# Kernel optimization log

Measured on AMD Instinct MI355X. Metric: run time of the kernel, lower is better.

The kernel has to match this reference:

```python
import jax, jax.numpy as jnp
import numpy as np

NA = 40000   # author nodes
NP = 40000   # paper nodes
E = 800000   # edges per relation
HID = 64
HOP = 5
SEM = 128


def setup_inputs() -> dict:
    key = jax.random.key(0)
    ks = jax.random.split(key, 32)
    f32 = jnp.float32
    rn = lambda k, s, sc=0.1: jax.random.normal(k, s, f32) * sc
    inp = {}
    inp["x_author"] = jax.random.normal(ks[0], (NA, 334), f32)
    inp["x_paper"] = jax.random.normal(ks[1], (NP, 512), f32)
    inp["W1_a"] = rn(ks[2], (334, HID), 0.05)
    inp["b1_a"] = jnp.zeros((HID,), f32)
    inp["W1_p"] = rn(ks[3], (512, HID), 0.05)
    inp["b1_p"] = jnp.zeros((HID,), f32)
    inp["a1_ap"] = rn(ks[4], (HOP, HID))
    inp["a2_ap"] = rn(ks[5], (HOP, HID))
    inp["a1_aa"] = rn(ks[6], (HOP, HID))
    inp["a2_aa"] = rn(ks[7], (HOP, HID))
    inp["a1_pa"] = rn(ks[8], (HOP, HID))
    inp["a2_pa"] = rn(ks[9], (HOP, HID))
    inp["a1_pp"] = rn(ks[10], (HOP, HID))
    inp["a2_pp"] = rn(ks[11], (HOP, HID))
    inp["semW_a"] = rn(ks[12], (HOP, HID, SEM))
    inp["semb_a"] = jnp.zeros((HOP, SEM), f32)
    inp["semq_a"] = rn(ks[13], (HOP, SEM))
    inp["semW_p"] = rn(ks[14], (HOP, HID, SEM))
    inp["semb_p"] = jnp.zeros((HOP, SEM), f32)
    inp["semq_p"] = rn(ks[15], (HOP, SEM))
    inp["W2"] = rn(ks[16], (HID, 4))
    inp["b2"] = jnp.zeros((4,), f32)
    inp["ei_ap"] = jax.random.randint(ks[17], (2, E), 0, NA)  # row0=src(author) row1=tgt(paper)
    inp["ei_aa"] = jax.random.randint(ks[18], (2, E), 0, NA)
    inp["ei_pa"] = jax.random.randint(ks[19], (2, E), 0, NP)
    inp["ei_pp"] = jax.random.randint(ks[20], (2, E), 0, NP)
    return inp


def _leaky(v):
    return jnp.where(v > 0.0, v, 0.2 * v)


def _edge_agg(x, h, s, t, a1, a2, n):
    # x: [Ns,D] source features (fixed), h: [Nt,D] current target state
    x1 = x @ a1                                   # [Ns]
    h1 = h @ a2                                   # [Nt]
    w2 = jnp.exp(_leaky(x1 + x @ a2))             # [Ns] self-loop score
    w1 = jnp.exp(_leaky(x1[s] + h1[t]))           # [E]  edge score
    div = jax.ops.segment_sum(w1, s, num_segments=n) + w2
    num = jax.ops.segment_sum(w1[:, None] * h[t], s, num_segments=n) + w2[:, None] * x
    return num / div[:, None]


def _sem(z, W, b, q):
    # z: [N,M,D]; HAN-style semantic attention over M relations
    sc = jnp.tanh(jnp.einsum('nmd,dk->nmk', z, W) + b) @ q   # [N,M]
    beta = jax.nn.softmax(jnp.mean(sc, axis=0))               # [M]
    return jnp.einsum('m,nmd->nd', beta, z)


def reference(x_author, x_paper, W1_a, b1_a, W1_p, b1_p,
              a1_ap, a2_ap, a1_aa, a2_aa, a1_pa, a2_pa, a1_pp, a2_pp,
              semW_a, semb_a, semq_a, semW_p, semb_p, semq_p,
              W2, b2, ei_ap, ei_aa, ei_pa, ei_pp):
    # eval mode: dropout is identity
    xA = jax.nn.relu(x_author @ W1_a + b1_a)
    xP = jax.nn.relu(x_paper @ W1_p + b1_p)
    hA, hP = xA, xP
    nA, nP = xA.shape[0], xP.shape[0]
    for i in range(HOP):
        eA = jnp.stack([
            _edge_agg(xA, hP, ei_ap[0], ei_ap[1], a1_ap[i], a2_ap[i], nA),
            _edge_agg(xA, hA, ei_aa[0], ei_aa[1], a1_aa[i], a2_aa[i], nA)], axis=1)
        eP = jnp.stack([
            _edge_agg(xP, hA, ei_pa[0], ei_pa[1], a1_pa[i], a2_pa[i], nP),
            _edge_agg(xP, hP, ei_pp[0], ei_pp[1], a1_pp[i], a2_pp[i], nP)], axis=1)
        hA = jax.nn.elu(_sem(eA, semW_a[i], semb_a[i], semq_a[i]))
        hP = jax.nn.elu(_sem(eP, semW_p[i], semb_p[i], semq_p[i]))
    return hA @ W2 + b2   # target_node_type = 'author'
```

## Files before the change

### kernel.cpp

```cpp
#include <hip/hip_runtime.h>
#include <hip/hip_fp16.h>

#define NN 40000
#define DD 64
#define EE 800000
#define NHOP 5
#define NSEM 128
#define NBK 625
#define BINCH 8192

__device__ __forceinline__ float leaky02(float v) { return v > 0.f ? v : 0.2f * v; }
__device__ __forceinline__ float tanh_fast(float x) {
  return 1.f - 2.f / (__expf(2.f * x) + 1.f);
}
__device__ __forceinline__ float wred(float x) {
  #pragma unroll
  for (int m = 1; m < 64; m <<= 1) x += __shfl_xor(x, m);
  return x;
}

__global__ void zero_i32(int* __restrict__ p, int n) {
  int i = blockIdx.x * blockDim.x + threadIdx.x;
  if (i < n) p[i] = 0;
}

#define PBM 64
#define PBK 64
__global__ __launch_bounds__(512) void proj_gemm_relu(
    const float* __restrict__ X, const float* __restrict__ W,
    const float* __restrict__ bias, float* __restrict__ out,
    __half* __restrict__ out16, int n, int K)
{
  __shared__ float As[PBM][PBK + 1];
  __shared__ float Bs[PBK][DD];
  int tid = threadIdx.x;
  int tx = tid & 15;
  int ty = tid >> 4;
  int row0 = blockIdx.x * PBM;
  float acc[2][4] = {{0.f}};
  int nk = (K + PBK - 1) / PBK;
  for (int kt = 0; kt < nk; ++kt) {
    int k0 = kt * PBK;
    #pragma unroll
    for (int j = 0; j < 8; ++j) {
      int idx = tid + j * 512;
      int r = idx >> 6, c = idx & 63;
      int gk = k0 + c;
      As[r][c] = (gk < K) ? X[(size_t)(row0 + r) * K + gk] : 0.f;
    }
    #pragma unroll
    for (int j = 0; j < 2; ++j) {
      int idx = tid + j * 512;
      int r = idx >> 4, c4 = idx & 15;
      int gk = k0 + r;
      float4 v = (gk < K) ? ((const float4*)(W + (size_t)gk * DD))[c4]
                          : make_float4(0.f, 0.f, 0.f, 0.f);
      ((float4*)&Bs[r][0])[c4] = v;
    }
    __syncthreads();
    #pragma unroll 8
    for (int kk = 0; kk < PBK; ++kk) {
      float a0 = As[ty * 2][kk];
      float a1 = As[ty * 2 + 1][kk];
      float4 bv = ((float4*)&Bs[kk][0])[tx];
      acc[0][0] = fmaf(a0, bv.x, acc[0][0]);
      acc[0][1] = fmaf(a0, bv.y, acc[0][1]);
      acc[0][2] = fmaf(a0, bv.z, acc[0][2]);
      acc[0][3] = fmaf(a0, bv.w, acc[0][3]);
      acc[1][0] = fmaf(a1, bv.x, acc[1][0]);
      acc[1][1] = fmaf(a1, bv.y, acc[1][1]);
      acc[1][2] = fmaf(a1, bv.z, acc[1][2]);
      acc[1][3] = fmaf(a1, bv.w, acc[1][3]);
    }
    __syncthreads();
  }
  float4 bb = ((const float4*)bias)[tx];
  #pragma unroll
  for (int i = 0; i < 2; ++i) {
    int gr = row0 + ty * 2 + i;
    float4 v;
    v.x = fmaxf(acc[i][0] + bb.x, 0.f);
    v.y = fmaxf(acc[i][1] + bb.y, 0.f);
    v.z = fmaxf(acc[i][2] + bb.z, 0.f);
    v.w = fmaxf(acc[i][3] + bb.w, 0.f);
    ((float4*)(out + (size_t)gr * DD))[tx] = v;
    __half2 p0 = __floats2half2_rn(v.x, v.y);
    __half2 p1 = __floats2half2_rn(v.z, v.w);
    ((__half2*)(out16 + (size_t)gr * DD))[tx * 2 + 0] = p0;
    ((__half2*)(out16 + (size_t)gr * DD))[tx * 2 + 1] = p1;
  }
}

__global__ __launch_bounds__(256) void binCount_kernel(
    const int* __restrict__ e0, const int* __restrict__ e1,
    const int* __restrict__ e2, const int* __restrict__ e3,
    int* __restrict__ bcnt, int e)
{
  int rel = blockIdx.y;
  const int* S = rel == 0 ? e0 : rel == 1 ? e1 : rel == 2 ? e2 : e3;
  __shared__ int cnt[NBK];
  int tid = threadIdx.x;
  for (int b = tid; b < NBK; b += 256) cnt[b] = 0;
  __syncthreads();
  int e0i = blockIdx.x * BINCH;
  int ne = min(BINCH, e - e0i);
  for (int i = tid; i < ne; i += 256) atomicAdd(&cnt[S[e0i + i] >> 6], 1);
  __syncthreads();
  for (int b = tid; b < NBK; b += 256)
    if (cnt[b]) atomicAdd(&bcnt[rel * NBK + b], cnt[b]);
}

__global__ __launch_bounds__(1024) void bucketScan_kernel(
    const int* __restrict__ bcnt, int* __restrict__ bbase, int* __restrict__ bcur,
    int* __restrict__ rp0, int* __restrict__ rp1, int* __restrict__ rp2,
    int* __restrict__ rp3, int e)
{
  int rel = blockIdx.x;
  __shared__ int sh[1024];
  int t = threadIdx.x;
  int v = (t < NBK) ? bcnt[rel * NBK + t] : 0;
  sh[t] = v;
  __syncthreads();
  for (int off = 1; off < 1024; off <<= 1) {
    int y = (t >= off) ? sh[t - off] : 0;
    __syncthreads();
    sh[t] += y;
    __syncthreads();
  }
  if (t < NBK) {
    int base = sh[t] - v;
    bbase[rel * (NBK + 1) + t] = base;
    bcur[rel * NBK + t] = base;
  }
  if (t == 0) {
    bbase[rel * (NBK + 1) + NBK] = e;
    (rel == 0 ? rp0 : rel == 1 ? rp1 : rel == 2 ? rp2 : rp3)[NN] = e;
  }
}

__global__ __launch_bounds__(256) void binA_kernel(
    const int* __restrict__ e0, const int* __restrict__ e1,
    const int* __restrict__ e2, const int* __restrict__ e3,
    int* __restrict__ bcur, unsigned* __restrict__ pairbuf, int e)
{
  int rel = blockIdx.y;
  const int* S = rel == 0 ? e0 : rel == 1 ? e1 : rel == 2 ? e2 : e3;
  const int* T = S + e;
  unsigned* pb = pairbuf + (size_t)rel * e;
  __shared__ int cnt[NBK], base[NBK], cnt2[NBK];
  int tid = threadIdx.x;
  for (int b = tid; b < NBK; b += 256) { cnt[b] = 0; cnt2[b] = 0; }
  __syncthreads();
  int e0i = blockIdx.x * BINCH;
  int ne = min(BINCH, e - e0i);
  for (int i = tid; i < ne; i += 256) atomicAdd(&cnt[S[e0i + i] >> 6], 1);
  __syncthreads();
  for (int b = tid; b < NBK; b += 256)
    base[b] = cnt[b] ? atomicAdd(&bcur[rel * NBK + b], cnt[b]) : 0;
  __syncthreads();
  for (int i = tid; i < ne; i += 256) {
    int s = S[e0i + i];
    int t = T[e0i + i];
    int b = s >> 6;
    int off = atomicAdd(&cnt2[b], 1);
    pb[base[b] + off] = ((unsigned)(s & 63) << 16) | (unsigned)t;
  }
}

__global__ __launch_bounds__(256) void binB_kernel(
    const unsigned* __restrict__ pairbuf, const int* __restrict__ bbase,
    int* __restrict__ rp0, int* __restrict__ rp1, int* __restrict__ rp2,
    int* __restrict__ rp3,
    unsigned short* __restrict__ ts0, unsigned short* __restrict__ ts1,
    unsigned short* __restrict__ ts2, unsigned short* __restrict__ ts3, int e)
{
  int rel = blockIdx.y;
  int* rowptr = rel == 0 ? rp0 : rel == 1 ? rp1 : rel == 2 ? rp2 : rp3;
  unsigned short* ts = rel == 0 ? ts0 : rel == 1 ? ts1 : rel == 2 ? ts2 : ts3;
  const unsigned* pb = pairbuf + (size_t)rel * e;
  int b = blockIdx.x;
  int bstart = bbase[rel * (NBK + 1) + b];
  int bend   = bbase[rel * (NBK + 1) + b + 1];
  __shared__ int ncnt[64], cur[64];
  int tid = threadIdx.x;
  if (tid < 64) ncnt[tid] = 0;
  __syncthreads();
  for (int i = bstart + tid; i < bend; i += 256)
    atomicAdd(&ncnt[(pb[i] >> 16) & 63], 1);
  __syncthreads();
  if (tid < 64) {
    int v = ncnt[tid];
    int x = v;
    #pragma unroll
    for (int off = 1; off < 64; off <<= 1) {
      int y = __shfl_up(x, off);
      if (tid >= off) x += y;
    }
    int nb = bstart + x - v;
    rowptr[b * 64 + tid] = nb;
    cur[tid] = nb;
  }
  __syncthreads();
  for (int i = bstart + tid; i < bend; i += 256) {
    unsigned u = pb[i];
    int pos = atomicAdd(&cur[(u >> 16) & 63], 1);
    ts[pos] = (unsigned short)(u & 0xffffu);
  }
}

__global__ __launch_bounds__(256) void precompute_xw(
    const float* __restrict__ xA, const float* __restrict__ xP,
    const float* __restrict__ a1_ap, const float* __restrict__ a2_ap,
    const float* __restrict__ a1_aa, const float* __restrict__ a2_aa,
    const float* __restrict__ a1_pa, const float* __restrict__ a2_pa,
    const float* __restrict__ a1_pp, const float* __restrict__ a2_pp,
    float* __restrict__ x1all, float* __restrict__ w2all,
    float* __restrict__ h1_ap, float* __restrict__ h1_aa,
    float* __restrict__ h1_pa, float* __restrict__ h1_pp)
{
  int side = blockIdx.y;
  __shared__ float L[21 * DD];
  int tid = threadIdx.x;
  {
    const float* s0 = side ? a1_pa : a1_ap;
    const float* s1 = side ? a2_pa : a2_ap;
    const float* s2 = side ? a1_pp : a1_aa;
    const float* s3 = side ? a2_pp : a2_aa;
    const float* ex = side ? a2_ap : a2_pa;
    for (int i = tid; i < 21 * DD; i += 256) {
      int k = i >> 6, d = i & 63;
      const float* src = (k < 5) ? s0 : (k < 10) ? s1 : (k < 15) ? s2 : (k < 20) ? s3 : ex;
      int hop = (k < 20) ? (k % 5) : 0;
      L[i] = src[hop * DD + d];
    }
  }
  __syncthreads();
  int j = blockIdx.x * 256 + tid;
  if (j >= NN) return;
  const float4* x4 = (const float4*)((side ? xP : xA) + (size_t)j * DD);
  float acc[21];
  #pragma unroll
  for (int k = 0; k < 21; ++k) acc[k] = 0.f;
  #pragma unroll
  for (int d0 = 0; d0 < 16; ++d0) {
    float4 v = x4[d0];
    #pragma unroll
    for (int c = 0; c < 4; ++c) {
      int d = d0 * 4 + c;
      float xv = (&v.x)[c];
      #pragma unroll
      for (int k = 0; k < 21; ++k) acc[k] = fmaf(xv, L[k * DD + d], acc[k]);
    }
  }
  int relA = side ? 2 : 0;
  #pragma unroll
  for (int i = 0; i < NHOP; ++i) {
    x1all[((size_t)(relA + 0) * NHOP + i) * NN + j] = acc[0 * 5 + i];
    w2all[((size_t)(relA + 0) * NHOP + i) * NN + j] =
        __expf(leaky02(acc[0 * 5 + i] + acc[1 * 5 + i]));
    x1all[((size_t)(relA + 1) * NHOP + i) * NN + j] = acc[2 * 5 + i];
    w2all[((size_t)(relA + 1) * NHOP + i) * NN + j] =
        __expf(leaky02(acc[2 * 5 + i] + acc[3 * 5 + i]));
  }
  if (side) { h1_pp[j] = acc[15]; h1_ap[j] = acc[20]; }
  else      { h1_aa[j] = acc[15]; h1_pa[j] = acc[20]; }
}

struct AggRel {
  const float* x; const __half2* h2; const float* x1; const float* w2; const float* h1;
  const int* rowptr; const unsigned short* tsorted; float* out;
};

__global__ __launch_bounds__(256) void agg4_kernel(AggRel r0, AggRel r1, AggRel r2,
                                                   AggRel r3, int n)
{
  int bid = blockIdx.x;
  int g = (bid >> 2) & 1;
  int u = (bid >> 3) * 4 + (bid & 3);
  int half = n >> 2;
  int relsel = u >= half;
  int nodeblk = relsel ? (u - half) : u;
  AggRel R;
  if (g == 0) R = relsel ? r2 : r1;
  else        R = relsel ? r3 : r0;

  int wid = nodeblk * 4 + (threadIdx.x >> 6);
  int lane = threadIdx.x & 63;
  int pair = lane >> 5;
  int c2 = lane & 31;

  int beg = R.rowptr[wid], end = R.rowptr[wid + 1];
  float x1i = R.x1[wid];
  float2 accA = make_float2(0.f, 0.f), accB = make_float2(0.f, 0.f);
  float2 accC = make_float2(0.f, 0.f), accD = make_float2(0.f, 0.f);
  float wsumL = 0.f;
  for (int c = beg; c < end; c += 64) {
    int idx = c + lane;
    int t = 0;
    float wv = 0.f;
    if (idx < end) {
      t = R.tsorted[idx];
      wv = __expf(leaky02(x1i + R.h1[t]));
    }
    wsumL += wv;
    int ne = min(64, end - c);
    for (int j = 0; j < ne; j += 8) {
      int s0 = j + pair, s1 = j + 2 + pair, s2 = j + 4 + pair, s3 = j + 6 + pair;
      int t0 = __shfl(t, s0), t1 = __shfl(t, s1);
      int t2 = __shfl(t, s2), t3 = __shfl(t, s3);
      float w0 = __shfl(wv, s0), w1 = __shfl(wv, s1);
      float w2_ = __shfl(wv, s2), w3 = __shfl(wv, s3);
      float2 f0 = __half22float2(R.h2[((unsigned)t0 << 5) + c2]);
      float2 f1 = __half22float2(R.h2[((unsigned)t1 << 5) + c2]);
      float2 f2 = __half22float2(R.h2[((unsigned)t2 << 5) + c2]);
      float2 f3 = __half22float2(R.h2[((unsigned)t3 << 5) + c2]);
      accA.x = fmaf(w0, f0.x, accA.x);
      accA.y = fmaf(w0, f0.y, accA.y);
      accB.x = fmaf(w1, f1.x, accB.x);
      accB.y = fmaf(w1, f1.y, accB.y);
      accC.x = fmaf(w2_, f2.x, accC.x);
      accC.y = fmaf(w2_, f2.y, accC.y);
      accD.x = fmaf(w3, f3.x, accD.x);
      accD.y = fmaf(w3, f3.y, accD.y);
    }
  }
  float wsum = wred(wsumL);
  float2 acc;
  acc.x = (accA.x + accB.x) + (accC.x + accD.x);
  acc.y = (accA.y + accB.y) + (accC.y + accD.y);
  acc.x += __shfl_xor(acc.x, 32);
  acc.y += __shfl_xor(acc.y, 32);
  if (pair == 0) {
    float w2v = R.w2[wid];
    float inv = 1.f / (wsum + w2v);
    float2 xv = ((const float2*)(R.x + (size_t)wid * DD))[c2];
    float2 o;
    o.x = fmaf(w2v, xv.x, acc.x) * inv;
    o.y = fmaf(w2v, xv.y, acc.y) * inv;
    ((float2*)(R.out + (size_t)wid * DD))[c2] = o;
  }
}

__global__ __launch_bounds__(256) void sem_kernel(
    const float* __restrict__ eA0, const float* __restrict__ eA1,
    const float* __restrict__ eP0, const float* __restrict__ eP1,
    const float* __restrict__ Wa, const float* __restrict__ ba, const float* __restrict__ qa,
    const float* __restrict__ Wp, const float* __restrict__ bp, const float* __restrict__ qp,
    float* __restrict__ psums)
{
  int side = blockIdx.y;
  const float* e0 = side ? eP0 : eA0;
  const float* e1 = side ? eP1 : eA1;
  const float* W = side ? Wp : Wa;
  const float* b = side ? bp : ba;
  const float* q = side ? qp : qa;

  __shared__ float Ws[DD * NSEM];
  __shared__ float zt[2][DD][12];
  __shared__ float red0[256], red1[256];
  int tid = threadIdx.x;
  {
    const float4* W4 = (const float4*)W;
    float4* Ws4 = (float4*)Ws;
    #pragma unroll
    for (int j = 0; j < 8; ++j) Ws4[tid + j * 256] = W4[tid + j * 256];
  }
  int slot = tid >> 7;
  int k = tid & 127;
  float bk = b[k], qk = q[k];
  int base = blockIdx.x * 64;
  float sum0 = 0.f, sum1 = 0.f;
  for (int it = 0; it < 8; ++it) {
    #pragma unroll
    for (int j = 0; j < 4; ++j) {
      int idx = tid + j * 256;
      int d = idx & 63, m = (idx >> 6) & 1, nn = idx >> 7;
      zt[m][d][nn] = (m ? e1 : e0)[(size_t)(base + it * 8 + nn) * DD + d];
    }
    __syncthreads();
    float a0[4], a1[4];
    #pragma unroll
    for (int nn = 0; nn < 4; ++nn) { a0[nn] = bk; a1[nn] = bk; }
    #pragma unroll 8
    for (int d = 0; d < DD; ++d) {
      float w = Ws[d * NSEM + k];
      float4 za = *(const float4*)&zt[0][d][slot * 4];
      float4 zb = *(const float4*)&zt[1][d][slot * 4];
      a0[0] = fmaf(za.x, w, a0[0]);
      a0[1] = fmaf(za.y, w, a0[1]);
      a0[2] = fmaf(za.z, w, a0[2]);
      a0[3] = fmaf(za.w, w, a0[3]);
      a1[0] = fmaf(zb.x, w, a1[0]);
      a1[1] = fmaf(zb.y, w, a1[1]);
      a1[2] = fmaf(zb.z, w, a1[2]);
      a1[3] = fmaf(zb.w, w, a1[3]);
    }
    #pragma unroll
    for (int nn = 0; nn < 4; ++nn) {
      sum0 += tanh_fast(a0[nn]) * qk;
      sum1 += tanh_fast(a1[nn]) * qk;
    }
    __syncthreads();
  }
  red0[tid] = sum0;
  red1[tid] = sum1;
  __syncthreads();
  for (int off = 128; off; off >>= 1) {
    if (tid < off) { red0[tid] += red0[tid + off]; red1[tid] += red1[tid + off]; }
    __syncthreads();
  }
  if (tid == 0) {
    int idx = (side * gridDim.x + blockIdx.x) * 2;
    psums[idx + 0] = red0[0];
    psums[idx + 1] = red1[0];
  }
}

__global__ __launch_bounds__(256) void beta_kernel(const float* __restrict__ psums,
    float* __restrict__ beta, int nblk, float invn)
{
  __shared__ float s[4][256];
  int t = threadIdx.x;
  float a0 = 0.f, a1 = 0.f, p0 = 0.f, p1 = 0.f;
  for (int i = t; i < nblk; i += 256) {
    a0 += psums[i * 2];
    a1 += psums[i * 2 + 1];
    p0 += psums[(nblk + i) * 2];
    p1 += psums[(nblk + i) * 2 + 1];
  }
  s[0][t] = a0; s[1][t] = a1; s[2][t] = p0; s[3][t] = p1;
  __syncthreads();
  for (int off = 128; off; off >>= 1) {
    if (t < off) {
      s[0][t] += s[0][t + off]; s[1][t] += s[1][t + off];
      s[2][t] += s[2][t + off]; s[3][t] += s[3][t + off];
    }
    __syncthreads();
  }
  if (t == 0) {
    float m0 = s[0][0] * invn, m1 = s[1][0] * invn;
    float mx = fmaxf(m0, m1);
    float x0 = __expf(m0 - mx), x1 = __expf(m1 - mx);
    float inv = 1.f / (x0 + x1);
    beta[0] = x0 * inv; beta[1] = x1 * inv;
    m0 = s[2][0] * invn; m1 = s[3][0] * invn;
    mx = fmaxf(m0, m1);
    x0 = __expf(m0 - mx); x1 = __expf(m1 - mx);
    inv = 1.f / (x0 + x1);
    beta[2] = x0 * inv; beta[3] = x1 * inv;
  }
}

__global__ void combine2_kernel(const float4* __restrict__ eA0, const float4* __restrict__ eA1,
    const float4* __restrict__ eP0, const float4* __restrict__ eP1,
    const float* __restrict__ beta, float4* __restrict__ hA, float4* __restrict__ hP,
    __half2* __restrict__ hA16, __half2* __restrict__ hP16,
    const float* __restrict__ a2_ap_n, const float* __restrict__ a2_aa_n,
    const float* __restrict__ a2_pa_n, const float* __restrict__ a2_pp_n,
    float* __restrict__ h1_ap, float* __restrict__ h1_aa,
    float* __restrict__ h1_pa, float* __restrict__ h1_pp,
    int has_next, int nvec)
{
  int side = blockIdx.y;
  int i = blockIdx.x * 256 + threadIdx.x;
  if (i >= nvec) return;
  float b0 = beta[side * 2], b1 = beta[side * 2 + 1];
  float4 v0 = (side ? eP0 : eA0)[i];
  float4 v1 = (side ? eP1 : eA1)[i];
  float4 r;
  float t;
  t = b0 * v0.x + b1 * v1.x; r.x = t > 0.f ? t : (__expf(t) - 1.f);
  t = b0 * v0.y + b1 * v1.y; r.y = t > 0.f ? t : (__expf(t) - 1.f);
  t = b0 * v0.z + b1 * v1.z; r.z = t > 0.f ? t : (__expf(t) - 1.f);
  t = b0 * v0.w + b1 * v1.w; r.w = t > 0.f ? t : (__expf(t) - 1.f);
  (side ? hP : hA)[i] = r;
  (side ? hP16 : hA16)[i * 2 + 0] = __floats2half2_rn(r.x, r.y);
  (side ? hP16 : hA16)[i * 2 + 1] = __floats2half2_rn(r.z, r.w);
  if (has_next) {
    int col4 = i & 15;
    const float* ax = side ? a2_ap_n : a2_aa_n;
    const float* ay = side ? a2_pp_n : a2_pa_n;
    float4 a4 = ((const float4*)ax)[col4];
    float4 c4 = ((const float4*)ay)[col4];
    float rx = r.x * a4.x + r.y * a4.y + r.z * a4.z + r.w * a4.w;
    float ry = r.x * c4.x + r.y * c4.y + r.z * c4.z + r.w * c4.w;
    #pragma unroll
    for (int m = 1; m < 16; m <<= 1) {
      rx += __shfl_xor(rx, m);
      ry += __shfl_xor(ry, m);
    }
    if ((threadIdx.x & 15) == 0) {
      int row = i >> 4;
      if (side) { h1_ap[row] = rx; h1_pp[row] = ry; }
      else      { h1_aa[row] = rx; h1_pa[row] = ry; }
    }
  }
}

__global__ void final_kernel(const float* __restrict__ hA, const float* __restrict__ W2,
    const float* __restrict__ b2, float* __restrict__ out, int n)
{
  int j = blockIdx.x * blockDim.x + threadIdx.x;
  if (j >= n) return;
  float acc0 = b2[0], acc1 = b2[1], acc2 = b2[2], acc3 = b2[3];
  const float4* hrow = (const float4*)(hA + (size_t)j * DD);
  #pragma unroll
  for (int d4 = 0; d4 < 16; ++d4) {
    float4 v = hrow[d4];
    #pragma unroll
    for (int c = 0; c < 4; ++c) {
      int d = d4 * 4 + c;
      float vv = (&v.x)[c];
      acc0 = fmaf(vv, W2[d * 4 + 0], acc0);
      acc1 = fmaf(vv, W2[d * 4 + 1], acc1);
      acc2 = fmaf(vv, W2[d * 4 + 2], acc2);
      acc3 = fmaf(vv, W2[d * 4 + 3], acc3);
    }
  }
  ((float4*)out)[j] = make_float4(acc0, acc1, acc2, acc3);
}

extern "C" void kernel_launch(void* const* d_in, const int* in_sizes, int n_in,
                              void* d_out, int out_size, void* d_ws, size_t ws_size,
                              hipStream_t stream)
{
  const float* x_author = (const float*)d_in[0];
  const float* x_paper  = (const float*)d_in[1];
  const float* W1_a = (const float*)d_in[2];
  const float* b1_a = (const float*)d_in[3];
  const float* W1_p = (const float*)d_in[4];
  const float* b1_p = (const float*)d_in[5];
  const float* a1_ap = (const float*)d_in[6];
  const float* a2_ap = (const float*)d_in[7];
  const float* a1_aa = (const float*)d_in[8];
  const float* a2_aa = (const float*)d_in[9];
  const float* a1_pa = (const float*)d_in[10];
  const float* a2_pa = (const float*)d_in[11];
  const float* a1_pp = (const float*)d_in[12];
  const float* a2_pp = (const float*)d_in[13];
  const float* semW_a = (const float*)d_in[14];
  const float* semb_a = (const float*)d_in[15];
  const float* semq_a = (const float*)d_in[16];
  const float* semW_p = (const float*)d_in[17];
  const float* semb_p = (const float*)d_in[18];
  const float* semq_p = (const float*)d_in[19];
  const float* W2 = (const float*)d_in[20];
  const float* b2 = (const float*)d_in[21];
  const int* ei[4] = {(const int*)d_in[22], (const int*)d_in[23],
                      (const int*)d_in[24], (const int*)d_in[25]};

  char* w = (char*)d_ws;
  auto alloc = [&](size_t bytes) -> void* {
    void* p = (void*)w;
    w += (bytes + 255) & ~(size_t)255;
    return p;
  };
  const size_t matB = (size_t)NN * DD * sizeof(float);
  float* xA  = (float*)alloc(matB);
  float* xP  = (float*)alloc(matB);
  float* hA  = (float*)alloc(matB);
  float* hP  = (float*)alloc(matB);
  float* eA0 = (float*)alloc(matB);
  float* eA1 = (float*)alloc(matB);
  float* eP0 = (float*)alloc(matB);
  float* eP1 = (float*)alloc(matB);
  __half* xA16 = (__half*)alloc(matB / 2);
  __half* xP16 = (__half*)alloc(matB / 2);
  __half* hA16 = xA16;
  __half* hP16 = xP16;
  unsigned* pairbuf = (unsigned*)eA0;
  int* rowptr[4]; unsigned short* tsorted[4];
  for (int r = 0; r < 4; ++r) {
    rowptr[r]  = (int*)alloc((NN + 1) * sizeof(int));
    tsorted[r] = (unsigned short*)alloc((size_t)EE * sizeof(unsigned short));
  }
  int* bcnt  = (int*)alloc((size_t)4 * NBK * sizeof(int));
  int* bbase = (int*)alloc((size_t)4 * (NBK + 1) * sizeof(int));
  int* bcur  = (int*)alloc((size_t)4 * NBK * sizeof(int));
  float* x1all = (float*)alloc((size_t)4 * NHOP * NN * sizeof(float));
  float* w2all = (float*)alloc((size_t)4 * NHOP * NN * sizeof(float));
  float* h1b[4];
  for (int r = 0; r < 4; ++r) h1b[r] = (float*)alloc(NN * sizeof(float));
  float* psums = (float*)alloc((size_t)2 * NBK * 2 * sizeof(float));
  float* betab = (float*)alloc(64);

  proj_gemm_relu<<<NN / PBM, 512, 0, stream>>>(x_author, W1_a, b1_a, xA, xA16, NN, 334);
  proj_gemm_relu<<<NN / PBM, 512, 0, stream>>>(x_paper,  W1_p, b1_p, xP, xP16, NN, 512);

  const int NEB = (EE + BINCH - 1) / BINCH;
  zero_i32<<<(4 * NBK + 255) / 256, 256, 0, stream>>>(bcnt, 4 * NBK);
  binCount_kernel<<<dim3(NEB, 4), 256, 0, stream>>>(ei[0], ei[1], ei[2], ei[3], bcnt, EE);
  bucketScan_kernel<<<4, 1024, 0, stream>>>(bcnt, bbase, bcur,
      rowptr[0], rowptr[1], rowptr[2], rowptr[3], EE);
  binA_kernel<<<dim3(NEB, 4), 256, 0, stream>>>(
      ei[0], ei[1], ei[2], ei[3], bcur, pairbuf, EE);
  binB_kernel<<<dim3(NBK, 4), 256, 0, stream>>>(pairbuf, bbase,
      rowptr[0], rowptr[1], rowptr[2], rowptr[3],
      tsorted[0], tsorted[1], tsorted[2], tsorted[3], EE);

  precompute_xw<<<dim3((NN + 255) / 256, 2), 256, 0, stream>>>(
      xA, xP, a1_ap, a2_ap, a1_aa, a2_aa, a1_pa, a2_pa, a1_pp, a2_pp,
      x1all, w2all, h1b[0], h1b[1], h1b[2], h1b[3]);

  const int CVEC = NN * DD / 4;
  for (int i = 0; i < NHOP; ++i) {
    #define X1(r) (x1all + ((size_t)(r) * NHOP + i) * NN)
    #define W2P(r) (w2all + ((size_t)(r) * NHOP + i) * NN)
    AggRel r0 = {xA, (const __half2*)hP16, X1(0), W2P(0), h1b[0], rowptr[0], tsorted[0], eA0};
    AggRel r1 = {xA, (const __half2*)hA16, X1(1), W2P(1), h1b[1], rowptr[1], tsorted[1], eA1};
    AggRel r2 = {xP, (const __half2*)hA16, X1(2), W2P(2), h1b[2], rowptr[2], tsorted[2], eP0};
    AggRel r3 = {xP, (const __half2*)hP16, X1(3), W2P(3), h1b[3], rowptr[3], tsorted[3], eP1};
    agg4_kernel<<<NN, 256, 0, stream>>>(r0, r1, r2, r3, NN);

    sem_kernel<<<dim3(NN / 64, 2), 256, 0, stream>>>(
        eA0, eA1, eP0, eP1,
        semW_a + (size_t)i * DD * NSEM, semb_a + i * NSEM, semq_a + i * NSEM,
        semW_p + (size_t)i * DD * NSEM, semb_p + i * NSEM, semq_p + i * NSEM,
        psums);
    beta_kernel<<<1, 256, 0, stream>>>(psums, betab, NN / 64, 1.f / NN);

    int inext = (i + 1 < NHOP) ? (i + 1) : i;
    combine2_kernel<<<dim3((CVEC + 255) / 256, 2), 256, 0, stream>>>(
        (const float4*)eA0, (const float4*)eA1, (const float4*)eP0, (const float4*)eP1,
        betab, (float4*)hA, (float4*)hP, (__half2*)hA16, (__half2*)hP16,
        a2_ap + inext * DD, a2_aa + inext * DD, a2_pa + inext * DD, a2_pp + inext * DD,
        h1b[0], h1b[1], h1b[2], h1b[3], (i + 1 < NHOP) ? 1 : 0, CVEC);
  }

  final_kernel<<<(NN + 255) / 256, 256, 0, stream>>>(hA, W2, b2, (float*)d_out, NN);
}
```

Before: 988.2 us.

## Replace tiled projection GEMM with thread-per-row kernel merging both node types

The shared-memory tiled projection GEMM is replaced by a kernel where each thread computes one full 64-wide output row. The thread reads its input row with vector loads and reads W rows as broadcast loads. Both author and paper projections now run in a single launch over a 2D grid. This drops LDS staging and a launch, but each thread streams its own strided row of X with no coalescing across threads and holds 64 accumulators, so memory efficiency and occupancy may suffer.

```diff
diff --git a/kernel.cpp b/kernel.cpp
--- a/kernel.cpp
+++ b/kernel.cpp
@@ -24,71 +24,64 @@
   if (i < n) p[i] = 0;
 }
 
-#define PBM 64
-#define PBK 64
-__global__ __launch_bounds__(512) void proj_gemm_relu(
+template <int VEC>
+__device__ __forceinline__ void proj_tpn_body(
     const float* __restrict__ X, const float* __restrict__ W,
     const float* __restrict__ bias, float* __restrict__ out,
-    __half* __restrict__ out16, int n, int K)
-{
-  __shared__ float As[PBM][PBK + 1];
-  __shared__ float Bs[PBK][DD];
-  int tid = threadIdx.x;
-  int tx = tid & 15;
-  int ty = tid >> 4;
-  int row0 = blockIdx.x * PBM;
-  float acc[2][4] = {{0.f}};
-  int nk = (K + PBK - 1) / PBK;
-  for (int kt = 0; kt < nk; ++kt) {
-    int k0 = kt * PBK;
-    #pragma unroll
-    for (int j = 0; j < 8; ++j) {
-      int idx = tid + j * 512;
-      int r = idx >> 6, c = idx & 63;
-      int gk = k0 + c;
-      As[r][c] = (gk < K) ? X[(size_t)(row0 + r) * K + gk] : 0.f;
-    }
-    #pragma unroll
-    for (int j = 0; j < 2; ++j) {
-      int idx = tid + j * 512;
-      int r = idx >> 4, c4 = idx & 15;
-      int gk = k0 + r;
-      float4 v = (gk < K) ? ((const float4*)(W + (size_t)gk * DD))[c4]
-                          : make_float4(0.f, 0.f, 0.f, 0.f);
-      ((float4*)&Bs[r][0])[c4] = v;
-    }
-    __syncthreads();
-    #pragma unroll 8
-    for (int kk = 0; kk < PBK; ++kk) {
-      float a0 = As[ty * 2][kk];
-      float a1 = As[ty * 2 + 1][kk];
-      float4 bv = ((float4*)&Bs[kk][0])[tx];
-      acc[0][0] = fmaf(a0, bv.x, acc[0][0]);
-      acc[0][1] = fmaf(a0, bv.y, acc[0][1]);
-      acc[0][2] = fmaf(a0, bv.z, acc[0][2]);
-      acc[0][3] = fmaf(a0, bv.w, acc[0][3]);
-      acc[1][0] = fmaf(a1, bv.x, acc[1][0]);
-      acc[1][1] = fmaf(a1, bv.y, acc[1][1]);
-      acc[1][2] = fmaf(a1, bv.z, acc[1][2]);
-      acc[1][3] = fmaf(a1, bv.w, acc[1][3]);
-    }
-    __syncthreads();
-  }
-  float4 bb = ((const float4*)bias)[tx];
+    __half* __restrict__ out16, int K, int j)
+{
+  const float* xrow = X + (size_t)j * K;
+  float acc[DD];
   #pragma unroll
-  for (int i = 0; i < 2; ++i) {
-    int gr = row0 + ty * 2 + i;
+  for (int o = 0; o < DD; ++o) acc[o] = 0.f;
+  for (int k = 0; k < K; k += VEC) {
+    float xv[VEC];
+    if (VEC == 4) {
+      float4 t = *(const float4*)(xrow + k);
+      xv[0] = t.x; xv[1] = t.y; xv[2] = t.z; xv[3] = t.w;
+    } else {
+      float2 t = *(const float2*)(xrow + k);
+      xv[0] = t.x; xv[1] = t.y;
+    }
+    #pragma unroll
+    for (int c = 0; c < VEC; ++c) {
+      const float4* wrow = (const float4*)(W + (size_t)(k + c) * DD);
+      #pragma unroll
+      for (int o4 = 0; o4 < 16; ++o4) {
+        float4 wv = wrow[o4];
+        acc[o4 * 4 + 0] = fmaf(xv[c], wv.x, acc[o4 * 4 + 0]);
+        acc[o4 * 4 + 1] = fmaf(xv[c], wv.y, acc[o4 * 4 + 1]);
+        acc[o4 * 4 + 2] = fmaf(xv[c], wv.z, acc[o4 * 4 + 2]);
+        acc[o4 * 4 + 3] = fmaf(xv[c], wv.w, acc[o4 * 4 + 3]);
+      }
+    }
+  }
+  float* orow = out + (size_t)j * DD;
+  __half2* orow16 = (__half2*)(out16 + (size_t)j * DD);
+  #pragma unroll
+  for (int o4 = 0; o4 < 16; ++o4) {
+    float4 bb = ((const float4*)bias)[o4];
     float4 v;
-    v.x = fmaxf(acc[i][0] + bb.x, 0.f);
-    v.y = fmaxf(acc[i][1] + bb.y, 0.f);
-    v.z = fmaxf(acc[i][2] + bb.z, 0.f);
-    v.w = fmaxf(acc[i][3] + bb.w, 0.f);
-    ((float4*)(out + (size_t)gr * DD))[tx] = v;
-    __half2 p0 = __floats2half2_rn(v.x, v.y);
-    __half2 p1 = __floats2half2_rn(v.z, v.w);
-    ((__half2*)(out16 + (size_t)gr * DD))[tx * 2 + 0] = p0;
-    ((__half2*)(out16 + (size_t)gr * DD))[tx * 2 + 1] = p1;
-  }
+    v.x = fmaxf(acc[o4 * 4 + 0] + bb.x, 0.f);
+    v.y = fmaxf(acc[o4 * 4 + 1] + bb.y, 0.f);
+    v.z = fmaxf(acc[o4 * 4 + 2] + bb.z, 0.f);
+    v.w = fmaxf(acc[o4 * 4 + 3] + bb.w, 0.f);
+    ((float4*)orow)[o4] = v;
+    orow16[o4 * 2 + 0] = __floats2half2_rn(v.x, v.y);
+    orow16[o4 * 2 + 1] = __floats2half2_rn(v.z, v.w);
+  }
+}
+
+__global__ __launch_bounds__(256) void proj_tpn_kernel(
+    const float* __restrict__ xa, const float* __restrict__ Wa,
+    const float* __restrict__ ba, float* __restrict__ oa, __half* __restrict__ oa16,
+    const float* __restrict__ xp, const float* __restrict__ Wp,
+    const float* __restrict__ bp, float* __restrict__ op, __half* __restrict__ op16)
+{
+  int j = blockIdx.x * 256 + threadIdx.x;
+  if (j >= NN) return;
+  if (blockIdx.y == 0) proj_tpn_body<2>(xa, Wa, ba, oa, oa16, 334, j);
+  else                 proj_tpn_body<4>(xp, Wp, bp, op, op16, 512, j);
 }
 
 __global__ __launch_bounds__(256) void binCount_kernel(
@@ -584,8 +577,9 @@
   float* psums = (float*)alloc((size_t)2 * NBK * 2 * sizeof(float));
   float* betab = (float*)alloc(64);
 
-  proj_gemm_relu<<<NN / PBM, 512, 0, stream>>>(x_author, W1_a, b1_a, xA, xA16, NN, 334);
-  proj_gemm_relu<<<NN / PBM, 512, 0, stream>>>(x_paper,  W1_p, b1_p, xP, xP16, NN, 512);
+  proj_tpn_kernel<<<dim3((NN + 255) / 256, 2), 256, 0, stream>>>(
+      x_author, W1_a, b1_a, xA, xA16,
+      x_paper,  W1_p, b1_p, xP, xP16);
 
   const int NEB = (EE + BINCH - 1) / BINCH;
   zero_i32<<<(4 * NBK + 255) / 256, 256, 0, stream>>>(bcnt, 4 * NBK);
```

Measured after the change: 1.042 ms. +5.4%, slower.
